# Kernel tuning notes

Hardware: AMD Instinct MI355X
Metric: run time of the kernel (lower is better)

The kernel has to match this reference:

```python
import jax, jax.numpy as jnp
import numpy as np

FT_IN = 40960   # HalfKP-style feature space
FFT_IN = 640    # factorized piece-square features
FT_OUT = 256


def setup_inputs() -> dict:
    key = jax.random.key(0)
    ks = jax.random.split(key, 10)
    B, A = 16384, 30  # batch, active features per board
    inp = {
        "stm_idx": jax.random.randint(ks[0], (B, A), 0, FT_IN, dtype=jnp.int32),
        "nstm_idx": jax.random.randint(ks[1], (B, A), 0, FT_IN, dtype=jnp.int32),
        "f_stm_idx": jax.random.randint(ks[2], (B, A), 0, FFT_IN, dtype=jnp.int32),
        "f_nstm_idx": jax.random.randint(ks[3], (B, A), 0, FFT_IN, dtype=jnp.int32),
        # learned parameters (glorot-ish scale)
        "ft_w": jax.random.normal(ks[4], (FT_IN, FT_OUT), jnp.float32) * 0.01,
        "ft_b": jax.random.normal(ks[5], (FT_OUT,), jnp.float32) * 0.01,
        "fft_w": jax.random.normal(ks[6], (FFT_IN, FT_OUT), jnp.float32) * 0.05,
        "fft_b": jax.random.normal(ks[7], (FT_OUT,), jnp.float32) * 0.01,
        "out_w": jax.random.normal(ks[8], (2 * FT_OUT, 1), jnp.float32) * 0.05,
        "out_b": jax.random.normal(ks[9], (1,), jnp.float32) * 0.01,
    }
    return inp


def _accumulate(w, b, idx):
    # sparse one-hot board @ kernel + bias == gather rows and sum over active features
    return jnp.take(w, idx, axis=0).sum(axis=1) + b  # [B, FT_OUT]


def reference(stm_idx, nstm_idx, f_stm_idx, f_nstm_idx,
              ft_w, ft_b, fft_w, fft_b, out_w, out_b):
    stm = _accumulate(ft_w, ft_b, stm_idx)        # [B, 256]
    nstm = _accumulate(ft_w, ft_b, nstm_idx)      # [B, 256]
    f_stm = _accumulate(fft_w, fft_b, f_stm_idx)  # [B, 256]
    f_nstm = _accumulate(fft_w, fft_b, f_nstm_idx)
    merge = jnp.concatenate((stm, nstm), axis=1) + jnp.concatenate((f_stm, f_nstm), axis=1)
    h = jnp.clip(merge, 0.0, 1.0)                 # ReLU(max_value=1.0)
    return jax.nn.sigmoid(h @ out_w + out_b)      # [B, 1]
```

## Files before the change

### kernel.cpp

```cpp
#include <hip/hip_runtime.h>
#include <math.h>

#define FT_IN  40960
#define FFT_IN 640
#define FT_OUT 256
#define NA     30
#define NSLICE 8
#define BPB    128
#define FTD    5
#define IDP    8

typedef _Float16 h2 __attribute__((ext_vector_type(2)));

__device__ __forceinline__ h2 u2h2(unsigned u) {
    union { unsigned u; h2 h; } c; c.u = u; return c.h;
}
__device__ __forceinline__ unsigned pkh(float a, float b) {
    union { h2 h; unsigned u; } c; c.h = h2{(_Float16)a, (_Float16)b}; return c.u;
}

__device__ __forceinline__ void conv_block(const float* __restrict__ src,
                                           unsigned* __restrict__ dst,
                                           int nrows, int bid, int tid)
{
    int t = bid * 256 + tid;
    int total = nrows * 32;
    if (t >= total) return;
    int r = t >> 5, g = t & 31;
    int s = g >> 2, d = g & 3;
    const float4* sp = (const float4*)(src + (size_t)r * FT_OUT + g * 8);
    float4 v0 = sp[0], v1 = sp[1];
    uint4 u;
    u.x = pkh(v0.x, v0.y); u.y = pkh(v0.z, v0.w);
    u.z = pkh(v1.x, v1.y); u.w = pkh(v1.z, v1.w);
    ((uint4*)dst)[((size_t)s * nrows + r) * 4 + d] = u;
}

__global__ __launch_bounds__(256) void prep(
    const float* __restrict__ ft_w, const float* __restrict__ fft_w,
    const int* __restrict__ stm, const int* __restrict__ nstm,
    const int* __restrict__ fstm, const int* __restrict__ fnstm,
    unsigned* __restrict__ ft_o, unsigned* __restrict__ fft_o,
    ushort4* __restrict__ pidx, int n_boards, int nb_ft, int nb_fft)
{
    int bid = blockIdx.x;
    if (bid < nb_ft) {
        conv_block(ft_w, ft_o, FT_IN, bid, threadIdx.x);
    } else if (bid < nb_ft + nb_fft) {
        conv_block(fft_w, fft_o, FFT_IN, bid - nb_ft, threadIdx.x);
    } else {
        int t = (bid - nb_ft - nb_fft) * 256 + (int)threadIdx.x;
        int total = n_boards * NA;
        if (t < total) {
            int board = t / NA, a = t - board * NA;
            ushort4 v;
            v.x = (unsigned short)stm[t];  v.y = (unsigned short)nstm[t];
            v.z = (unsigned short)fstm[t]; v.w = (unsigned short)fnstm[t];
            pidx[(size_t)a * n_boards + board] = v;
        }
    }
}

__global__ __launch_bounds__(512, 6) void nnue_gather(
    const unsigned long long* __restrict__ pidx,
    const char* __restrict__ ft, const char* __restrict__ fft,
    const float* __restrict__ ft_b, const float* __restrict__ fft_b,
    const float* __restrict__ out_w, float* __restrict__ partial, int n_boards)
{
    __shared__ uint4 lfft[FFT_IN * 4];
    const int slice = blockIdx.x & (NSLICE - 1);
    const int group = blockIdx.x >> 3;
    const int tid = (int)threadIdx.x;

    {
        const uint4* fsrc = (const uint4*)(fft + (size_t)slice * FFT_IN * 64);
        for (int i = tid; i < FFT_IN * 4; i += 512)
            lfft[i] = fsrc[i];
    }
    __syncthreads();

    const int sub = tid >> 2, ql = tid & 3;
    int board = group * BPB + sub;
    const bool active = board < n_boards;
    if (!active) board = n_boards - 1;

    const char* ftS = ft + (size_t)slice * FT_IN * 64 + ql * 16;
    const int col = slice * 32 + ql * 8;

    h2 z = h2{(_Float16)0.f, (_Float16)0.f};
    h2 a0[4] = {z, z, z, z};
    h2 a1[4] = {z, z, z, z};

    unsigned long long iv[IDP];
    #pragma unroll
    for (int a = 0; a < IDP; ++a)
        iv[a] = pidx[(size_t)a * n_boards + board];

    uint4 fs[FTD], fn[FTD];
    #pragma unroll
    for (int a = 0; a < FTD; ++a) {
        unsigned lo = (unsigned)iv[a];
        fs[a] = *(const uint4*)(ftS + ((lo & 0xFFFFu) << 6));
        fn[a] = *(const uint4*)(ftS + ((lo >> 16) << 6));
    }

    #pragma unroll
    for (int a = 0; a < NA; ++a) {
        const int k = a % FTD;
        const int j = a % IDP;
        unsigned hi = (unsigned)(iv[j] >> 32);
        unsigned rz = (hi & 0xFFFFu) << 2, rw = (hi >> 16) << 2;
        uint4 g0 = lfft[rz + ql];
        uint4 g1 = lfft[rw + ql];
        uint4 u0 = fs[k], u1 = fn[k];
        a0[0] += u2h2(u0.x); a0[1] += u2h2(u0.y); a0[2] += u2h2(u0.z); a0[3] += u2h2(u0.w);
        a1[0] += u2h2(u1.x); a1[1] += u2h2(u1.y); a1[2] += u2h2(u1.z); a1[3] += u2h2(u1.w);
        a0[0] += u2h2(g0.x); a0[1] += u2h2(g0.y); a0[2] += u2h2(g0.z); a0[3] += u2h2(g0.w);
        a1[0] += u2h2(g1.x); a1[1] += u2h2(g1.y); a1[2] += u2h2(g1.z); a1[3] += u2h2(g1.w);
        if (a + IDP < NA)
            iv[j] = pidx[(size_t)(a + IDP) * n_boards + board];
        if (a + FTD < NA) {
            unsigned lo = (unsigned)iv[(a + FTD) % IDP];
            fs[k] = *(const uint4*)(ftS + ((lo & 0xFFFFu) << 6));
            fn[k] = *(const uint4*)(ftS + ((lo >> 16) << 6));
        }
    }

    float h0[8], h1[8];
    #pragma unroll
    for (int i = 0; i < 4; ++i) {
        h0[2*i] = (float)a0[i].x; h0[2*i+1] = (float)a0[i].y;
        h1[2*i] = (float)a1[i].x; h1[2*i+1] = (float)a1[i].y;
    }
    const float4* bfp = (const float4*)(ft_b  + col);
    const float4* bgp = (const float4*)(fft_b + col);
    float4 bf0 = bfp[0], bf1 = bfp[1], bg0 = bgp[0], bg1 = bgp[1];
    float bias[8] = {bf0.x+bg0.x, bf0.y+bg0.y, bf0.z+bg0.z, bf0.w+bg0.w,
                     bf1.x+bg1.x, bf1.y+bg1.y, bf1.z+bg1.z, bf1.w+bg1.w};
    const float4* w0p = (const float4*)(out_w + col);
    const float4* w1p = (const float4*)(out_w + FT_OUT + col);
    float4 w00 = w0p[0], w01 = w0p[1], w10 = w1p[0], w11 = w1p[1];
    float w0[8] = {w00.x, w00.y, w00.z, w00.w, w01.x, w01.y, w01.z, w01.w};
    float w1[8] = {w10.x, w10.y, w10.z, w10.w, w11.x, w11.y, w11.z, w11.w};

    float p = 0.f;
    #pragma unroll
    for (int i = 0; i < 8; ++i) {
        p += fminf(fmaxf(h0[i] + bias[i], 0.f), 1.f) * w0[i];
        p += fminf(fmaxf(h1[i] + bias[i], 0.f), 1.f) * w1[i];
    }
    p += __shfl_xor(p, 1, 64);
    p += __shfl_xor(p, 2, 64);
    if (active && ql == 0) partial[(size_t)slice * n_boards + board] = p;
}

__global__ __launch_bounds__(256) void nnue_final(
    const float* __restrict__ partial, const float* __restrict__ out_b,
    float* __restrict__ out, int n)
{
    int b = blockIdx.x * blockDim.x + threadIdx.x;
    if (b >= n) return;
    float zv = out_b[0];
    #pragma unroll
    for (int s = 0; s < NSLICE; ++s) zv += partial[(size_t)s * n + b];
    out[b] = 1.0f / (1.0f + expf(-zv));
}

__global__ __launch_bounds__(256) void nnue_fwd_direct(
    const int* __restrict__ stm_idx, const int* __restrict__ nstm_idx,
    const int* __restrict__ f_stm_idx, const int* __restrict__ f_nstm_idx,
    const float* __restrict__ ft_w, const float* __restrict__ ft_b,
    const float* __restrict__ fft_w, const float* __restrict__ fft_b,
    const float* __restrict__ out_w, const float* __restrict__ out_b,
    float* __restrict__ out, int n_boards)
{
    const int board = (int)((blockIdx.x * blockDim.x + threadIdx.x) >> 6);
    const int lane  = (int)(threadIdx.x & 63);
    if (board >= n_boards) return;
    const int col = lane << 2;
    const float4 ftb  = *(const float4*)(ft_b  + col);
    const float4 fftb = *(const float4*)(fft_b + col);
    float a0x = ftb.x + fftb.x, a0y = ftb.y + fftb.y,
          a0z = ftb.z + fftb.z, a0w = ftb.w + fftb.w;
    float a1x = a0x, a1y = a0y, a1z = a0z, a1w = a0w;
    const int* si  = stm_idx    + (size_t)board * NA;
    const int* ni  = nstm_idx   + (size_t)board * NA;
    const int* fsi = f_stm_idx  + (size_t)board * NA;
    const int* fni = f_nstm_idx + (size_t)board * NA;
    #pragma unroll 5
    for (int a = 0; a < NA; ++a) {
        const float4 r0 = *(const float4*)(ft_w  + (size_t)si[a]  * FT_OUT + col);
        const float4 r1 = *(const float4*)(ft_w  + (size_t)ni[a]  * FT_OUT + col);
        const float4 r2 = *(const float4*)(fft_w + (size_t)fsi[a] * FT_OUT + col);
        const float4 r3 = *(const float4*)(fft_w + (size_t)fni[a] * FT_OUT + col);
        a0x += r0.x + r2.x; a0y += r0.y + r2.y; a0z += r0.z + r2.z; a0w += r0.w + r2.w;
        a1x += r1.x + r3.x; a1y += r1.y + r3.y; a1z += r1.z + r3.z; a1w += r1.w + r3.w;
    }
    a0x = fminf(fmaxf(a0x, 0.f), 1.f); a0y = fminf(fmaxf(a0y, 0.f), 1.f);
    a0z = fminf(fmaxf(a0z, 0.f), 1.f); a0w = fminf(fmaxf(a0w, 0.f), 1.f);
    a1x = fminf(fmaxf(a1x, 0.f), 1.f); a1y = fminf(fmaxf(a1y, 0.f), 1.f);
    a1z = fminf(fmaxf(a1z, 0.f), 1.f); a1w = fminf(fmaxf(a1w, 0.f), 1.f);
    const float4 w0 = *(const float4*)(out_w + col);
    const float4 w1 = *(const float4*)(out_w + FT_OUT + col);
    float p = a0x * w0.x + a0y * w0.y + a0z * w0.z + a0w * w0.w
            + a1x * w1.x + a1y * w1.y + a1z * w1.z + a1w * w1.w;
    #pragma unroll
    for (int off = 32; off > 0; off >>= 1) p += __shfl_down(p, off, 64);
    if (lane == 0) out[board] = 1.0f / (1.0f + expf(-(p + out_b[0])));
}

extern "C" void kernel_launch(void* const* d_in, const int* in_sizes, int n_in,
                              void* d_out, int out_size, void* d_ws, size_t ws_size,
                              hipStream_t stream) {
    const int*   stm_idx    = (const int*)d_in[0];
    const int*   nstm_idx   = (const int*)d_in[1];
    const int*   f_stm_idx  = (const int*)d_in[2];
    const int*   f_nstm_idx = (const int*)d_in[3];
    const float* ft_w  = (const float*)d_in[4];
    const float* ft_b  = (const float*)d_in[5];
    const float* fft_w = (const float*)d_in[6];
    const float* fft_b = (const float*)d_in[7];
    const float* out_w = (const float*)d_in[8];
    const float* out_b = (const float*)d_in[9];
    float* out = (float*)d_out;

    const int n_boards = in_sizes[0] / NA;

    const size_t ft_bytes   = (size_t)FT_IN  * FT_OUT * 2;
    const size_t fft_bytes  = (size_t)FFT_IN * FT_OUT * 2;
    const size_t pidx_bytes = (size_t)n_boards * NA * sizeof(ushort4);
    const size_t part_bytes = (size_t)n_boards * NSLICE * sizeof(float);
    const size_t need = ft_bytes + fft_bytes + pidx_bytes + part_bytes;

    if (ws_size < need) {
        const int grid = (n_boards + 3) / 4;
        nnue_fwd_direct<<<grid, 256, 0, stream>>>(stm_idx, nstm_idx, f_stm_idx, f_nstm_idx,
                                                  ft_w, ft_b, fft_w, fft_b, out_w, out_b,
                                                  out, n_boards);
        return;
    }

    char* wsp = (char*)d_ws;
    unsigned* ws_ft   = (unsigned*)wsp;            wsp += ft_bytes;
    unsigned* ws_fft  = (unsigned*)wsp;            wsp += fft_bytes;
    ushort4*  ws_pidx = (ushort4*)wsp;             wsp += pidx_bytes;
    float*    ws_part = (float*)wsp;

    {
        const int nb_ft   = FT_IN  * 32 / 256;
        const int nb_fft  = FFT_IN * 32 / 256;
        const int nb_pack = (n_boards * NA + 255) / 256;
        prep<<<nb_ft + nb_fft + nb_pack, 256, 0, stream>>>(
            ft_w, fft_w, stm_idx, nstm_idx, f_stm_idx, f_nstm_idx,
            ws_ft, ws_fft, ws_pidx, n_boards, nb_ft, nb_fft);
    }
    {
        int groups = (n_boards + BPB - 1) / BPB;
        nnue_gather<<<groups * NSLICE, 512, 0, stream>>>(
            (const unsigned long long*)ws_pidx, (const char*)ws_ft, (const char*)ws_fft,
            ft_b, fft_b, out_w, ws_part, n_boards);
    }
    {
        nnue_final<<<(n_boards + 255) / 256, 256, 0, stream>>>(ws_part, out_b, out, n_boards);
    }
}
```

Measured before the change: 148.4 us.

## Widen column slices to 128 bytes and stage per-board indices in LDS

Halves the number of column slices from 8 to 4, so each gathered fp16 row segment is 128 bytes read by 8 lanes per board, and blocks grow to 1024 threads. The packed indices for the block's 128 boards are preloaded cooperatively into dynamic shared memory. This replaces the software-pipelined register prefetch of indices and feature rows. The intent is fewer redundant index reads and wider, more coalesced gathers. In exchange it needs about 108 KB of dynamic LDS per block, which limits occupancy, and the explicit prefetch pipeline is lost.

```diff
diff --git a/kernel.cpp b/kernel.cpp
--- a/kernel.cpp
+++ b/kernel.cpp
@@ -5,12 +5,11 @@
 #define FFT_IN 640
 #define FT_OUT 256
 #define NA     30
-#define NSLICE 8
+#define NSLICE 4
 #define BPB    128
-#define FTD    5
-#define IDP    8
 
 typedef _Float16 h2 __attribute__((ext_vector_type(2)));
+typedef unsigned u32x4 __attribute__((ext_vector_type(4)));
 
 __device__ __forceinline__ h2 u2h2(unsigned u) {
     union { unsigned u; h2 h; } c; c.u = u; return c.h;
@@ -27,13 +26,13 @@
     int total = nrows * 32;
     if (t >= total) return;
     int r = t >> 5, g = t & 31;
-    int s = g >> 2, d = g & 3;
+    int s = g >> 3, d = g & 7;
     const float4* sp = (const float4*)(src + (size_t)r * FT_OUT + g * 8);
     float4 v0 = sp[0], v1 = sp[1];
     uint4 u;
     u.x = pkh(v0.x, v0.y); u.y = pkh(v0.z, v0.w);
     u.z = pkh(v1.x, v1.y); u.w = pkh(v1.z, v1.w);
-    ((uint4*)dst)[((size_t)s * nrows + r) * 4 + d] = u;
+    ((uint4*)dst)[((size_t)s * nrows + r) * 8 + d] = u;
 }
 
 __global__ __launch_bounds__(256) void prep(
@@ -61,69 +60,55 @@
     }
 }
 
-__global__ __launch_bounds__(512, 6) void nnue_gather(
-    const unsigned long long* __restrict__ pidx,
+__global__ __launch_bounds__(1024, 4) void nnue_gather(
+    const uint2* __restrict__ pidx,
     const char* __restrict__ ft, const char* __restrict__ fft,
     const float* __restrict__ ft_b, const float* __restrict__ fft_b,
     const float* __restrict__ out_w, float* __restrict__ partial, int n_boards)
 {
-    __shared__ uint4 lfft[FFT_IN * 4];
+    extern __shared__ char smem[];
+    uint2* lidx = (uint2*)smem;
+    u32x4* lfft = (u32x4*)(smem + NA * BPB * 8);
     const int slice = blockIdx.x & (NSLICE - 1);
-    const int group = blockIdx.x >> 3;
+    const int group = blockIdx.x >> 2;
     const int tid = (int)threadIdx.x;
 
-    {
-        const uint4* fsrc = (const uint4*)(fft + (size_t)slice * FFT_IN * 64);
-        for (int i = tid; i < FFT_IN * 4; i += 512)
+    for (int i = tid; i < NA * BPB; i += 1024) {
+        int b = i & (BPB - 1);
+        int bd = group * BPB + b;
+        uint2 v; v.x = 0u; v.y = 0u;
+        if (bd < n_boards) v = pidx[(size_t)(i >> 7) * n_boards + bd];
+        lidx[i] = v;
+    }
+    {
+        const u32x4* fsrc = (const u32x4*)(fft + (size_t)slice * FFT_IN * 128);
+        for (int i = tid; i < FFT_IN * 8; i += 1024)
             lfft[i] = fsrc[i];
     }
     __syncthreads();
 
-    const int sub = tid >> 2, ql = tid & 3;
+    const int sub = tid >> 3, ql = tid & 7;
     int board = group * BPB + sub;
     const bool active = board < n_boards;
-    if (!active) board = n_boards - 1;
-
-    const char* ftS = ft + (size_t)slice * FT_IN * 64 + ql * 16;
-    const int col = slice * 32 + ql * 8;
+    const unsigned qlo = (unsigned)(ql << 4);
+    const char* ftS = ft + (size_t)slice * FT_IN * 128 + qlo;
+    const int col = slice * 64 + ql * 8;
 
     h2 z = h2{(_Float16)0.f, (_Float16)0.f};
     h2 a0[4] = {z, z, z, z};
     h2 a1[4] = {z, z, z, z};
 
-    unsigned long long iv[IDP];
-    #pragma unroll
-    for (int a = 0; a < IDP; ++a)
-        iv[a] = pidx[(size_t)a * n_boards + board];
-
-    uint4 fs[FTD], fn[FTD];
-    #pragma unroll
-    for (int a = 0; a < FTD; ++a) {
-        unsigned lo = (unsigned)iv[a];
-        fs[a] = *(const uint4*)(ftS + ((lo & 0xFFFFu) << 6));
-        fn[a] = *(const uint4*)(ftS + ((lo >> 16) << 6));
-    }
-
     #pragma unroll
     for (int a = 0; a < NA; ++a) {
-        const int k = a % FTD;
-        const int j = a % IDP;
-        unsigned hi = (unsigned)(iv[j] >> 32);
-        unsigned rz = (hi & 0xFFFFu) << 2, rw = (hi >> 16) << 2;
-        uint4 g0 = lfft[rz + ql];
-        uint4 g1 = lfft[rw + ql];
-        uint4 u0 = fs[k], u1 = fn[k];
+        uint2 iv = lidx[a * BPB + sub];
+        u32x4 u0 = *(const u32x4*)(ftS + ((iv.x & 0xFFFFu) << 7));
+        u32x4 u1 = *(const u32x4*)(ftS + ((iv.x >> 16) << 7));
+        u32x4 g0 = lfft[((iv.y & 0xFFFFu) << 3) + ql];
+        u32x4 g1 = lfft[((iv.y >> 16) << 3) + ql];
         a0[0] += u2h2(u0.x); a0[1] += u2h2(u0.y); a0[2] += u2h2(u0.z); a0[3] += u2h2(u0.w);
         a1[0] += u2h2(u1.x); a1[1] += u2h2(u1.y); a1[2] += u2h2(u1.z); a1[3] += u2h2(u1.w);
         a0[0] += u2h2(g0.x); a0[1] += u2h2(g0.y); a0[2] += u2h2(g0.z); a0[3] += u2h2(g0.w);
         a1[0] += u2h2(g1.x); a1[1] += u2h2(g1.y); a1[2] += u2h2(g1.z); a1[3] += u2h2(g1.w);
-        if (a + IDP < NA)
-            iv[j] = pidx[(size_t)(a + IDP) * n_boards + board];
-        if (a + FTD < NA) {
-            unsigned lo = (unsigned)iv[(a + FTD) % IDP];
-            fs[k] = *(const uint4*)(ftS + ((lo & 0xFFFFu) << 6));
-            fn[k] = *(const uint4*)(ftS + ((lo >> 16) << 6));
-        }
     }
 
     float h0[8], h1[8];
@@ -151,7 +136,9 @@
     }
     p += __shfl_xor(p, 1, 64);
     p += __shfl_xor(p, 2, 64);
-    if (active && ql == 0) partial[(size_t)slice * n_boards + board] = p;
+    p += __shfl_xor(p, 4, 64);
+    if (active && ql == 0)
+        partial[(size_t)slice * n_boards + board] = p;
 }
 
 __global__ __launch_bounds__(256) void nnue_final(
@@ -232,7 +219,15 @@
     const size_t part_bytes = (size_t)n_boards * NSLICE * sizeof(float);
     const size_t need = ft_bytes + fft_bytes + pidx_bytes + part_bytes;
 
-    if (ws_size < need) {
+    const size_t lds_bytes = (size_t)NA * BPB * 8 + (size_t)FFT_IN * 128;
+
+    bool ok = (ws_size >= need);
+    if (ok) {
+        ok = (hipFuncSetAttribute((const void*)nnue_gather,
+                                  hipFuncAttributeMaxDynamicSharedMemorySize,
+                                  (int)lds_bytes) == hipSuccess);
+    }
+    if (!ok) {
         const int grid = (n_boards + 3) / 4;
         nnue_fwd_direct<<<grid, 256, 0, stream>>>(stm_idx, nstm_idx, f_stm_idx, f_nstm_idx,
                                                   ft_w, ft_b, fft_w, fft_b, out_w, out_b,
@@ -256,8 +251,8 @@
     }
     {
         int groups = (n_boards + BPB - 1) / BPB;
-        nnue_gather<<<groups * NSLICE, 512, 0, stream>>>(
-            (const unsigned long long*)ws_pidx, (const char*)ws_ft, (const char*)ws_fft,
+        nnue_gather<<<groups * NSLICE, 1024, lds_bytes, stream>>>(
+            (const uint2*)ws_pidx, (const char*)ws_ft, (const char*)ws_fft,
             ft_b, fft_b, out_w, ws_part, n_boards);
     }
     {
```

Result: faster. 139.4 us (-6.1%).
